# Optimization experiments

Hardware: AMD Instinct MI355X
Metric: run time of the kernel (lower is better)

The kernel has to match this reference:

```python
import jax, jax.numpy as jnp
import numpy as np

N_NODES = 1000
NODE_DIM = 40
SEQ_LEN = 12
IN_FEAT = 32
HID = 64
LAYERS = 3
GDEP = 2
TOPK = 20
TANH_ALPHA = 3.0
PROP_ALPHA = 0.05
LN_EPS = 1e-5


def setup_inputs() -> dict:
    key = jax.random.key(0)
    ks = jax.random.split(key, 20)
    s = 0.1  # weight init scale
    B = 64
    return {
        "x": jax.random.normal(ks[0], (B, N_NODES, SEQ_LEN, IN_FEAT), jnp.float32),
        # graph constructor params
        "emb1": jax.random.normal(ks[1], (N_NODES, NODE_DIM), jnp.float32) * s,
        "emb2": jax.random.normal(ks[2], (N_NODES, NODE_DIM), jnp.float32) * s,
        "lin1_w": jax.random.normal(ks[3], (NODE_DIM, NODE_DIM), jnp.float32) * s,
        "lin1_b": jnp.zeros((NODE_DIM,), jnp.float32),
        "lin2_w": jax.random.normal(ks[4], (NODE_DIM, NODE_DIM), jnp.float32) * s,
        "lin2_b": jnp.zeros((NODE_DIM,), jnp.float32),
        # LSTM (pytorch gate order i,f,g,o)
        "Wih": jax.random.normal(ks[5], (4 * HID, IN_FEAT), jnp.float32) * s,
        "Whh": jax.random.normal(ks[6], (4 * HID, HID), jnp.float32) * s,
        "bih": jnp.zeros((4 * HID,), jnp.float32),
        "bhh": jnp.zeros((4 * HID,), jnp.float32),
        # per-layer linear 64 -> seq_length
        "lin_w": jax.random.normal(ks[7], (LAYERS, SEQ_LEN, HID), jnp.float32) * s,
        "lin_b": jnp.zeros((LAYERS, SEQ_LEN), jnp.float32),
        # mixprop 1: (gdep+1)*12 -> 32
        "mp1_w": jax.random.normal(ks[8], (LAYERS, 32, (GDEP + 1) * SEQ_LEN), jnp.float32) * s,
        "mp1_b": jnp.zeros((LAYERS, 32), jnp.float32),
        # mixprop 2: (gdep+1)*32 -> node_dim
        "mp2_w": jax.random.normal(ks[9], (LAYERS, NODE_DIM, (GDEP + 1) * 32), jnp.float32) * s,
        "mp2_b": jnp.zeros((LAYERS, NODE_DIM), jnp.float32),
        # layernorm affine over (node_dim, N)
        "gamma": jnp.ones((LAYERS, NODE_DIM, N_NODES), jnp.float32),
        "beta": jnp.zeros((LAYERS, NODE_DIM, N_NODES), jnp.float32),
    }


def _graph_constructor(emb1, emb2, lin1_w, lin1_b, lin2_w, lin2_b):
    m1 = jnp.tanh(TANH_ALPHA * (emb1 @ lin1_w.T + lin1_b))
    m2 = jnp.tanh(TANH_ALPHA * (emb2 @ lin2_w.T + lin2_b))
    a = jax.nn.relu(jnp.tanh(TANH_ALPHA * (m1 @ m2.T - m2 @ m1.T)))
    _, idx = jax.lax.top_k(a, TOPK)  # keep top-k neighbors per row
    mask = jnp.zeros_like(a).at[jnp.arange(a.shape[0])[:, None], idx].set(1.0)
    return a * mask


def _lstm_last(x, Wih, Whh, bih, bhh):
    # x: (B, T, IN_FEAT) -> last hidden state (B, HID)
    B = x.shape[0]
    h0 = jnp.zeros((B, HID), x.dtype)
    c0 = jnp.zeros((B, HID), x.dtype)

    def step(carry, xt):
        h, c = carry
        g = xt @ Wih.T + h @ Whh.T + bih + bhh
        i, f, gg, o = jnp.split(g, 4, axis=-1)
        c = jax.nn.sigmoid(f) * c + jax.nn.sigmoid(i) * jnp.tanh(gg)
        h = jax.nn.sigmoid(o) * jnp.tanh(c)
        return (h, c), None

    (h, _), _ = jax.lax.scan(step, (h0, c0), jnp.swapaxes(x, 0, 1))
    return h


def _mixprop(h, adj_norm, w, b):
    # h: (B, C, N); adj_norm: (N, N) row-normalized (adj + I)
    x0 = h
    outs = [h]
    for _ in range(GDEP):
        h = PROP_ALPHA * x0 + (1.0 - PROP_ALPHA) * jnp.einsum('bcw,vw->bcv', h, adj_norm)
        outs.append(h)
    ho = jnp.concatenate(outs, axis=1)  # (B, C*(GDEP+1), N)
    return jnp.einsum('bcn,oc->bon', ho, w) + b[None, :, None]


def _layernorm(h, gamma, beta):
    # normalize over (C, N) dims
    mu = jnp.mean(h, axis=(1, 2), keepdims=True)
    var = jnp.var(h, axis=(1, 2), keepdims=True)
    return (h - mu) * jax.lax.rsqrt(var + LN_EPS) * gamma[None] + beta[None]


def reference(x, emb1, emb2, lin1_w, lin1_b, lin2_w, lin2_b,
              Wih, Whh, bih, bhh, lin_w, lin_b,
              mp1_w, mp1_b, mp2_w, mp2_b, gamma, beta):
    B, N, T, F = x.shape
    adj = _graph_constructor(emb1, emb2, lin1_w, lin1_b, lin2_w, lin2_b)
    adj = adj + jnp.eye(N, dtype=adj.dtype)
    adj_norm = adj / jnp.sum(adj, axis=1, keepdims=True)

    out = _lstm_last(x.reshape(B * N, T, F), Wih, Whh, bih, bhh)  # (B*N, 64)

    h = None
    for j in range(LAYERS):
        hj = out @ lin_w[j].T + lin_b[j]                # (B*N, 12)
        hj = hj.reshape(B, N, SEQ_LEN).transpose(0, 2, 1)  # (B, 12, N)
        hj = jax.nn.relu(_mixprop(hj, adj_norm, mp1_w[j], mp1_b[j]))
        # dropout is identity in eval mode
        hj = _mixprop(hj, adj_norm, mp2_w[j], mp2_b[j])  # (B, node_dim, N)
        h = _layernorm(hj, gamma[j], beta[j])

    return h.transpose(0, 2, 1).reshape(B, N * NODE_DIM)
```

## Files before the change

kernel.cpp:

```cpp
#include <hip/hip_runtime.h>


typedef unsigned short u16;
typedef __attribute__((ext_vector_type(8))) short bf16x8;
typedef __attribute__((ext_vector_type(4))) float fx4;

#define NB 64
#define NNODE 1000
#define TT 12
#define FF 32
#define HH 64
#define DD 40
#define TOPK_ 20
#define EPR2 22

__device__ __forceinline__ float rcp_f(float x) { return __builtin_amdgcn_rcpf(x); }
__device__ __forceinline__ float tanh_f(float x) {
  return fmaf(-2.0f, rcp_f(__expf(2.0f * x) + 1.0f), 1.0f);
}
__device__ __forceinline__ unsigned int cvt_pk(float lo, float hi) {
  unsigned int r;
  asm("v_cvt_pk_bf16_f32 %0, %1, %2" : "=v"(r) : "v"(lo), "v"(hi));
  return r;
}
__device__ __forceinline__ bf16x8 cvt8(const float* p) {
  union { unsigned int u[4]; bf16x8 v; } r;
  #pragma unroll
  for (int e = 0; e < 4; e++) r.u[e] = cvt_pk(p[2 * e], p[2 * e + 1]);
  return r.v;
}
__device__ __forceinline__ bf16x8 cvt8v(float4 a, float4 b) {
  union { unsigned int u[4]; bf16x8 v; } r;
  r.u[0] = cvt_pk(a.x, a.y); r.u[1] = cvt_pk(a.z, a.w);
  r.u[2] = cvt_pk(b.x, b.y); r.u[3] = cvt_pk(b.z, b.w);
  return r.v;
}

__global__ void k_m1m2(const float* __restrict__ emb1, const float* __restrict__ emb2,
                       const float* __restrict__ w1, const float* __restrict__ b1,
                       const float* __restrict__ w2, const float* __restrict__ b2,
                       float* __restrict__ m1, float* __restrict__ m2,
                       const float* __restrict__ lw, const float* __restrict__ lb,
                       const float* __restrict__ p1w, const float* __restrict__ p1b,
                       const float* __restrict__ p2w, const float* __restrict__ p2b,
                       float* __restrict__ wt) {
  int tid = threadIdx.x;
  if (blockIdx.x == 313) {
    for (int i = tid; i < 768; i += 256) { int k = i / 12, s = i % 12; wt[i] = lw[s * 64 + k]; }
    if (tid < 12) wt[768 + tid] = lb[tid];
    for (int i = tid; i < 1152; i += 256) { int c = i / 32, o = i % 32; wt[784 + i] = p1w[o * 36 + c]; }
    if (tid < 32) wt[1936 + tid] = p1b[tid];
    for (int i = tid; i < 3840; i += 256) { int c = i / 40, o = i % 40; wt[1968 + i] = p2w[o * 96 + c]; }
    if (tid < 40) wt[5808 + tid] = p2b[tid];
    return;
  }
  int id = blockIdx.x * 256 + tid;
  if (id >= 2 * NNODE * DD) return;
  int sel = id / (NNODE * DD);
  int r = id % (NNODE * DD);
  int i = r / DD, o = r % DD;
  const float4* emb = (const float4*)((sel ? emb2 : emb1) + i * DD);
  const float4* w = (const float4*)((sel ? w2 : w1) + o * DD);
  float s = (sel ? b2 : b1)[o];
  #pragma unroll
  for (int k4 = 0; k4 < DD / 4; k4++) {
    float4 a = emb[k4], b = w[k4];
    s = fmaf(a.x, b.x, s); s = fmaf(a.y, b.y, s);
    s = fmaf(a.z, b.z, s); s = fmaf(a.w, b.w, s);
  }
  (sel ? m2 : m1)[r] = tanh_f(3.0f * s);
}

__global__ void k_adj(const float* __restrict__ m1, const float* __restrict__ m2,
                      int2* __restrict__ pae) {
  int v0 = blockIdx.x * 4, tid = threadIdx.x;
  int lane = tid & 63, wave = tid >> 6;
  __shared__ float arow4[4][1024];
  __shared__ float m1v4[4][DD], m2v4[4][DD];
  for (int i = tid; i < 4 * DD; i += 256) {
    int r = i / DD, k = i % DD;
    m1v4[r][k] = m1[(v0 + r) * DD + k];
    m2v4[r][k] = m2[(v0 + r) * DD + k];
  }
  __syncthreads();
  for (int w = tid; w < NNODE; w += 256) {
    const float4* m2r = (const float4*)(m2 + w * DD);
    const float4* m1r = (const float4*)(m1 + w * DD);
    float4 a[10], bb[10];
    #pragma unroll
    for (int k4 = 0; k4 < 10; k4++) { a[k4] = m2r[k4]; bb[k4] = m1r[k4]; }
    #pragma unroll
    for (int r = 0; r < 4; r++) {
      float d1 = 0.f, d2 = 0.f;
      #pragma unroll
      for (int k4 = 0; k4 < 10; k4++) {
        d1 = fmaf(m1v4[r][k4 * 4 + 0], a[k4].x, d1);
        d1 = fmaf(m1v4[r][k4 * 4 + 1], a[k4].y, d1);
        d1 = fmaf(m1v4[r][k4 * 4 + 2], a[k4].z, d1);
        d1 = fmaf(m1v4[r][k4 * 4 + 3], a[k4].w, d1);
        d2 = fmaf(m2v4[r][k4 * 4 + 0], bb[k4].x, d2);
        d2 = fmaf(m2v4[r][k4 * 4 + 1], bb[k4].y, d2);
        d2 = fmaf(m2v4[r][k4 * 4 + 2], bb[k4].z, d2);
        d2 = fmaf(m2v4[r][k4 * 4 + 3], bb[k4].w, d2);
      }
      arow4[r][w] = fmaxf(tanh_f(3.0f * (d1 - d2)), 0.0f);
    }
  }
  __syncthreads();
  int v = v0 + wave, l = lane;
  float rv[16];
  #pragma unroll
  for (int q = 0; q < 16; q++) {
    int idx = q * 64 + l;
    rv[q] = (idx < NNODE) ? arow4[wave][idx] : -2.f;
  }
  float rs = 1.f;
  float myv = 0.f; int myi = 0;
  #pragma unroll
  for (int sel = 0; sel < TOPK_; sel++) {
    float bv = rv[0]; int bi = l;
    #pragma unroll
    for (int q = 1; q < 16; q++) {
      int idx = q * 64 + l;
      if (rv[q] > bv) { bv = rv[q]; bi = idx; }
    }
    #pragma unroll
    for (int off = 1; off < 64; off <<= 1) {
      float ov = __shfl_xor(bv, off); int oi = __shfl_xor(bi, off);
      if (ov > bv || (ov == bv && oi < bi)) { bv = ov; bi = oi; }
    }
    rs += bv;
    if (l == sel + 1) { myv = bv; myi = bi; }
    #pragma unroll
    for (int q = 0; q < 16; q++)
      if (q * 64 + l == bi) rv[q] = -2.f;
  }
  float inv = rcp_f(rs);
  if (l == 0)          pae[v * EPR2] = make_int2(v, __float_as_int(inv));
  else if (l <= TOPK_) pae[v * EPR2 + l] = make_int2(myi, __float_as_int(myv * inv));
  else if (l == 21)    pae[v * EPR2 + 21] = make_int2(v, 0);
}

__global__ __launch_bounds__(256, 3)
void k_lstm(const float* __restrict__ x, const float* __restrict__ Wih,
            const float* __restrict__ Whh, const float* __restrict__ bih,
            const float* __restrict__ bhh, const float* __restrict__ wt,
            float* __restrict__ hj) {
  __shared__ __align__(16) u16 whf[2 * 16 * 64 * 8];
  __shared__ __align__(16) u16 hsh[4][16][64];
  __shared__ float lwsh[12 * 64];
  __shared__ float lbsh[12];
  __shared__ float bsh[256];
  int tid = threadIdx.x, wave = tid >> 6, lane = tid & 63;
  int arow = lane & 15, kg = lane >> 4;

  for (int cc = tid; cc < 2 * 16 * 64; cc += 256) {
    int l = cc & 63, t16 = cc >> 6, ks = t16 >> 4, nt = t16 & 15;
    int row = (nt >> 2) * 64 + (l & 15) * 4 + (nt & 3);
    *(bf16x8*)&whf[cc * 8] = cvt8(Whh + row * 64 + ks * 32 + (l >> 4) * 8);
  }
  for (int i = tid; i < 768; i += 256) { int s = i >> 6, j = i & 63; lwsh[i] = wt[j * 12 + s]; }
  if (tid < 12) lbsh[tid] = wt[768 + tid];
  {
    int nt = tid >> 4, c = tid & 15;
    int row = (nt >> 2) * 64 + c * 4 + (nt & 3);
    bsh[tid] = bih[row] + bhh[row];
  }
  __syncthreads();

  bf16x8 wi[16];
  #pragma unroll
  for (int nt = 0; nt < 16; nt++) {
    int row = (nt >> 2) * 64 + arow * 4 + (nt & 3);
    wi[nt] = cvt8(Wih + row * 32 + kg * 8);
  }

  int seq_base = blockIdx.x * 64 + wave * 16;
  const float* xb = x + (size_t)(seq_base + arow) * (TT * FF) + kg * 8;
  float cst[16];
  #pragma unroll
  for (int q = 0; q < 16; q++) cst[q] = 0.f;

  float4 xf0 = *(const float4*)(xb);
  float4 xf1 = *(const float4*)(xb + 4);

  auto STEP = [&](int t, bool first, float (&hq)[16]) {
    unsigned int zo = 0;
    asm volatile("" : "+v"(zo));
    bf16x8 xa = cvt8v(xf0, xf1);
    if (t < TT - 1) {
      xf0 = *(const float4*)(xb + (t + 1) * FF);
      xf1 = *(const float4*)(xb + (t + 1) * FF + 4);
    }
    fx4 acc[16];
    #pragma unroll
    for (int nt = 0; nt < 16; nt++) {
      float bv = bsh[nt * 16 + arow];
      acc[nt] = (fx4){bv, bv, bv, bv};
    }
    #pragma unroll
    for (int nt = 0; nt < 16; nt++)
      acc[nt] = __builtin_amdgcn_mfma_f32_16x16x32_bf16(xa, wi[nt], acc[nt], 0, 0, 0);
    if (!first) {
      asm volatile("" ::: "memory");
      bf16x8 ha0 = *(const bf16x8*)&hsh[wave][arow][kg * 8];
      bf16x8 ha1 = *(const bf16x8*)&hsh[wave][arow][32 + kg * 8];
      asm volatile("" ::: "memory");
      #pragma unroll
      for (int nt = 0; nt < 16; nt++) {
        bf16x8 wb = *(const bf16x8*)&whf[(nt * 64 + lane) * 8 + zo];
        acc[nt] = __builtin_amdgcn_mfma_f32_16x16x32_bf16(ha0, wb, acc[nt], 0, 0, 0);
      }
      #pragma unroll
      for (int nt = 0; nt < 16; nt++) {
        bf16x8 wb = *(const bf16x8*)&whf[((16 + nt) * 64 + lane) * 8 + zo];
        acc[nt] = __builtin_amdgcn_mfma_f32_16x16x32_bf16(ha1, wb, acc[nt], 0, 0, 0);
      }
    }
    #pragma unroll
    for (int i = 0; i < 4; i++) {
      #pragma unroll
      for (int njt = 0; njt < 4; njt++) {
        float iv = acc[njt][i], fv = acc[njt + 4][i];
        float gv = acc[njt + 8][i], ov = acc[njt + 12][i];
        float cpv = cst[i * 4 + njt];
        float ei = __expf(-iv), ef = __expf(-fv);
        float eg = __expf(2.0f * gv), eo = __expf(-ov);
        float A = 1.0f + ef;
        float B = (1.0f + ei) * (eg + 1.0f);
        float c = fmaf(cpv, B, (eg - 1.0f) * A) * rcp_f(A * B);
        cst[i * 4 + njt] = c;
        float ec = __expf(2.0f * c);
        hq[i * 4 + njt] = (ec - 1.0f) * rcp_f((ec + 1.0f) * (1.0f + eo));
      }
    }
  };

  #pragma unroll 1
  for (int t = 0; t < TT - 1; t++) {
    float hq[16];
    STEP(t, t == 0, hq);
    #pragma unroll
    for (int i = 0; i < 4; i++) {
      unsigned int p0 = cvt_pk(hq[i * 4 + 0], hq[i * 4 + 1]);
      unsigned int p1 = cvt_pk(hq[i * 4 + 2], hq[i * 4 + 3]);
      *(uint2*)&hsh[wave][kg * 4 + i][arow * 4] = make_uint2(p0, p1);
    }
  }
  float hq[16];
  STEP(TT - 1, false, hq);

  #pragma unroll
  for (int i = 0; i < 4; i++) {
    float a[12];
    #pragma unroll
    for (int s = 0; s < 12; s++) a[s] = 0.f;
    #pragma unroll
    for (int njt = 0; njt < 4; njt++) {
      float hv = hq[i * 4 + njt];
      #pragma unroll
      for (int s = 0; s < 12; s++)
        a[s] = fmaf(hv, lwsh[s * 64 + arow * 4 + njt], a[s]);
    }
    #pragma unroll
    for (int off = 1; off < 16; off <<= 1) {
      #pragma unroll
      for (int s = 0; s < 12; s++) a[s] += __shfl_xor(a[s], off);
    }
    float outv = a[0];
    #pragma unroll
    for (int s = 1; s < 12; s++) outv = (arow == s) ? a[s] : outv;
    if (arow < 12) {
      int gseq = seq_base + kg * 4 + i;
      int bb = gseq / 1000, nn = gseq - bb * 1000;
      hj[(size_t)(bb * 12 + arow) * NNODE + nn] = outv + lbsh[arow];
    }
  }
}

__global__ void k_prop4(const float* __restrict__ hin, const int2* __restrict__ pae,
                        float* __restrict__ ho, int C) {
  int NG = C >> 2;
  int b = blockIdx.x / NG, g = blockIdx.x % NG;
  int c0 = g * 4;
  __shared__ __align__(16) float r0t[NNODE][4];
  __shared__ __align__(16) float r1t[NNODE][4];
  int tid = threadIdx.x;
  const float* src = hin + ((size_t)b * C + c0) * NNODE;
  float* dst = ho + (size_t)b * 2 * C * NNODE;
  for (int n = tid; n < NNODE; n += 256) {
    float4 v;
    v.x = src[n];
    v.y = src[NNODE + n];
    v.z = src[2 * NNODE + n];
    v.w = src[3 * NNODE + n];
    *(float4*)&r0t[n][0] = v;
  }
  __syncthreads();
  for (int n = tid; n < NNODE; n += 256) {
    const int4* pa4 = (const int4*)(pae + (size_t)n * EPR2);
    float4 s = {0.f, 0.f, 0.f, 0.f};
    #pragma unroll
    for (int e = 0; e < EPR2 / 2; e++) {
      int4 p = pa4[e];
      float av = __int_as_float(p.y);
      float4 rv = *(const float4*)&r0t[p.x][0];
      s.x = fmaf(av, rv.x, s.x); s.y = fmaf(av, rv.y, s.y);
      s.z = fmaf(av, rv.z, s.z); s.w = fmaf(av, rv.w, s.w);
      float aw = __int_as_float(p.w);
      float4 rw = *(const float4*)&r0t[p.z][0];
      s.x = fmaf(aw, rw.x, s.x); s.y = fmaf(aw, rw.y, s.y);
      s.z = fmaf(aw, rw.z, s.z); s.w = fmaf(aw, rw.w, s.w);
    }
    float4 x0 = *(const float4*)&r0t[n][0];
    float4 h1;
    h1.x = fmaf(0.95f, s.x, 0.05f * x0.x);
    h1.y = fmaf(0.95f, s.y, 0.05f * x0.y);
    h1.z = fmaf(0.95f, s.z, 0.05f * x0.z);
    h1.w = fmaf(0.95f, s.w, 0.05f * x0.w);
    *(float4*)&r1t[n][0] = h1;
    dst[(size_t)(c0 + 0) * NNODE + n] = h1.x;
    dst[(size_t)(c0 + 1) * NNODE + n] = h1.y;
    dst[(size_t)(c0 + 2) * NNODE + n] = h1.z;
    dst[(size_t)(c0 + 3) * NNODE + n] = h1.w;
  }
  __syncthreads();
  for (int n = tid; n < NNODE; n += 256) {
    const int4* pa4 = (const int4*)(pae + (size_t)n * EPR2);
    float4 s = {0.f, 0.f, 0.f, 0.f};
    #pragma unroll
    for (int e = 0; e < EPR2 / 2; e++) {
      int4 p = pa4[e];
      float av = __int_as_float(p.y);
      float4 rv = *(const float4*)&r1t[p.x][0];
      s.x = fmaf(av, rv.x, s.x); s.y = fmaf(av, rv.y, s.y);
      s.z = fmaf(av, rv.z, s.z); s.w = fmaf(av, rv.w, s.w);
      float aw = __int_as_float(p.w);
      float4 rw = *(const float4*)&r1t[p.z][0];
      s.x = fmaf(aw, rw.x, s.x); s.y = fmaf(aw, rw.y, s.y);
      s.z = fmaf(aw, rw.z, s.z); s.w = fmaf(aw, rw.w, s.w);
    }
    float4 x0 = *(const float4*)&r0t[n][0];
    dst[(size_t)(C + c0 + 0) * NNODE + n] = fmaf(0.95f, s.x, 0.05f * x0.x);
    dst[(size_t)(C + c0 + 1) * NNODE + n] = fmaf(0.95f, s.y, 0.05f * x0.y);
    dst[(size_t)(C + c0 + 2) * NNODE + n] = fmaf(0.95f, s.z, 0.05f * x0.z);
    dst[(size_t)(C + c0 + 3) * NNODE + n] = fmaf(0.95f, s.w, 0.05f * x0.w);
  }
}

template <int C1, int COUT>
__global__ void k_proj(const float* __restrict__ src0, const float* __restrict__ src12,
                       const float* __restrict__ wt, const float* __restrict__ bb,
                       float* __restrict__ out, int relu) {
  int id = blockIdx.x * 256 + threadIdx.x;
  int b = id / NNODE, n = id % NNODE;
  float acc[COUT];
  #pragma unroll
  for (int o = 0; o < COUT; o++) acc[o] = bb[o];
  for (int c = 0; c < C1; c++) {
    float hv = src0[(size_t)(b * C1 + c) * NNODE + n];
    #pragma unroll
    for (int o = 0; o < COUT; o++) acc[o] = fmaf(hv, wt[c * COUT + o], acc[o]);
  }
  for (int c = 0; c < 2 * C1; c++) {
    float hv = src12[(size_t)(b * 2 * C1 + c) * NNODE + n];
    #pragma unroll
    for (int o = 0; o < COUT; o++) acc[o] = fmaf(hv, wt[(C1 + c) * COUT + o], acc[o]);
  }
  #pragma unroll
  for (int o = 0; o < COUT; o++) {
    float vv = acc[o];
    if (relu) vv = fmaxf(vv, 0.f);
    out[(size_t)(b * COUT + o) * NNODE + n] = vv;
  }
}

__global__ void k_ln(const float* __restrict__ hj2, const float* __restrict__ gamma,
                     const float* __restrict__ beta, float* __restrict__ out) {
  int b = blockIdx.x, tid = threadIdx.x, lane = tid & 63, wave = tid >> 6;
  const float* base = hj2 + (size_t)b * DD * NNODE;
  const float4* p = (const float4*)base;
  float s = 0.f, q = 0.f;
  for (int i = tid; i < DD * NNODE / 4; i += 1024) {
    float4 vv = p[i];
    s += vv.x + vv.y + vv.z + vv.w;
    q = fmaf(vv.x, vv.x, q); q = fmaf(vv.y, vv.y, q);
    q = fmaf(vv.z, vv.z, q); q = fmaf(vv.w, vv.w, q);
  }
  for (int off = 32; off; off >>= 1) { s += __shfl_down(s, off); q += __shfl_down(q, off); }
  __shared__ float ss[16], sq[16];
  __shared__ float smu, srstd;
  if (lane == 0) { ss[wave] = s; sq[wave] = q; }
  __syncthreads();
  if (tid == 0) {
    const float invN = 1.0f / (float)(DD * NNODE);
    float S = 0.f, Q = 0.f;
    for (int t = 0; t < 16; t++) { S += ss[t]; Q += sq[t]; }
    float mu = S * invN;
    float var = Q * invN - mu * mu;
    smu = mu; srstd = __builtin_amdgcn_rsqf(var + 1e-5f);
  }
  __syncthreads();
  float mu = smu, rstd = srstd;
  if (tid >= NNODE) return;
  int n = tid;
  size_t obase = (size_t)b * (NNODE * DD) + (size_t)n * DD;
  #pragma unroll
  for (int d0 = 0; d0 < DD / 4; d0++) {
    float tt[4];
    #pragma unroll
    for (int qq = 0; qq < 4; qq++) {
      int d = d0 * 4 + qq;
      float h0 = base[(size_t)d * NNODE + n];
      tt[qq] = (h0 - mu) * rstd * gamma[d * NNODE + n] + beta[d * NNODE + n];
    }
    *(float4*)(out + obase + d0 * 4) = (float4){tt[0], tt[1], tt[2], tt[3]};
  }
}

#define OFF_M1   0
#define OFF_M2   40000
#define OFF_PAE  80000
#define OFF_HJ   124000
#define OFF_HO1  892000
#define OFF_O1   2428000
#define OFF_HO2  4476000
#define OFF_HJ2  8572000
#define OFF_WT   11132000

extern "C" void kernel_launch(void* const* d_in, const int* in_sizes, int n_in,
                              void* d_out, int out_size, void* d_ws, size_t ws_size,
                              hipStream_t stream) {
  (void)in_sizes; (void)n_in; (void)out_size; (void)ws_size;
  const float* x     = (const float*)d_in[0];
  const float* emb1  = (const float*)d_in[1];
  const float* emb2  = (const float*)d_in[2];
  const float* l1w   = (const float*)d_in[3];
  const float* l1b   = (const float*)d_in[4];
  const float* l2w   = (const float*)d_in[5];
  const float* l2b   = (const float*)d_in[6];
  const float* Wih   = (const float*)d_in[7];
  const float* Whh   = (const float*)d_in[8];
  const float* bih   = (const float*)d_in[9];
  const float* bhh   = (const float*)d_in[10];
  const float* lin_w = (const float*)d_in[11];
  const float* lin_b = (const float*)d_in[12];
  const float* mp1w  = (const float*)d_in[13];
  const float* mp1b  = (const float*)d_in[14];
  const float* mp2w  = (const float*)d_in[15];
  const float* mp2b  = (const float*)d_in[16];
  const float* gamma = (const float*)d_in[17];
  const float* beta  = (const float*)d_in[18];

  float* ws   = (float*)d_ws;
  float* m1   = ws + OFF_M1;
  float* m2   = ws + OFF_M2;
  int2*  pae  = (int2*)(ws + OFF_PAE);
  float* hj   = ws + OFF_HJ;
  float* ho1  = ws + OFF_HO1;
  float* o1   = ws + OFF_O1;
  float* ho2  = ws + OFF_HO2;
  float* hj2  = ws + OFF_HJ2;
  float* wt   = ws + OFF_WT;

  k_m1m2<<<dim3(314), dim3(256), 0, stream>>>(emb1, emb2, l1w, l1b, l2w, l2b, m1, m2,
                                              lin_w + 1536, lin_b + 24, mp1w + 2304,
                                              mp1b + 64, mp2w + 7680, mp2b + 80, wt);
  k_adj<<<dim3(250), dim3(256), 0, stream>>>(m1, m2, pae);
  k_lstm<<<dim3(1000), dim3(256), 0, stream>>>(x, Wih, Whh, bih, bhh, wt, hj);
  k_prop4<<<dim3(64 * 3), dim3(256), 0, stream>>>(hj, pae, ho1, 12);
  k_proj<12, 32><<<dim3(250), dim3(256), 0, stream>>>(hj, ho1, wt + 784, wt + 1936, o1, 1);
  k_prop4<<<dim3(64 * 8), dim3(256), 0, stream>>>(o1, pae, ho2, 32);
  k_proj<32, 40><<<dim3(250), dim3(256), 0, stream>>>(o1, ho2, wt + 1968, wt + 5808, hj2, 0);
  k_ln<<<dim3(NB), dim3(1024), 0, stream>>>(hj2, gamma + 80000, beta + 80000,
                                            (float*)d_out);
}
```

Measured before the change: 264.1 us.

## Fuse graph-embedding and weight-transpose prep into the LSTM kernel launch

The m1/m2 embedding projection and the mixprop weight transposes become extra blocks appended to the LSTM grid, which removes a separate launch and its serialization ahead of the LSTM. The LSTM now reads the lin weights directly instead of a pre-transposed copy, and it keeps the gate biases in registers rather than shared memory. Launch bounds drop from 3 to 2 blocks per CU, which lowers the occupancy target and may let the compiler allocate more registers. The adjacency kernel now runs after the fused kernel.

```diff
diff --git a/kernel.cpp b/kernel.cpp
--- a/kernel.cpp
+++ b/kernel.cpp
@@ -36,122 +36,50 @@
   return r.v;
 }
 
-__global__ void k_m1m2(const float* __restrict__ emb1, const float* __restrict__ emb2,
-                       const float* __restrict__ w1, const float* __restrict__ b1,
-                       const float* __restrict__ w2, const float* __restrict__ b2,
-                       float* __restrict__ m1, float* __restrict__ m2,
-                       const float* __restrict__ lw, const float* __restrict__ lb,
-                       const float* __restrict__ p1w, const float* __restrict__ p1b,
-                       const float* __restrict__ p2w, const float* __restrict__ p2b,
-                       float* __restrict__ wt) {
-  int tid = threadIdx.x;
-  if (blockIdx.x == 313) {
-    for (int i = tid; i < 768; i += 256) { int k = i / 12, s = i % 12; wt[i] = lw[s * 64 + k]; }
-    if (tid < 12) wt[768 + tid] = lb[tid];
-    for (int i = tid; i < 1152; i += 256) { int c = i / 32, o = i % 32; wt[784 + i] = p1w[o * 36 + c]; }
-    if (tid < 32) wt[1936 + tid] = p1b[tid];
-    for (int i = tid; i < 3840; i += 256) { int c = i / 40, o = i % 40; wt[1968 + i] = p2w[o * 96 + c]; }
-    if (tid < 40) wt[5808 + tid] = p2b[tid];
-    return;
-  }
-  int id = blockIdx.x * 256 + tid;
-  if (id >= 2 * NNODE * DD) return;
-  int sel = id / (NNODE * DD);
-  int r = id % (NNODE * DD);
-  int i = r / DD, o = r % DD;
-  const float4* emb = (const float4*)((sel ? emb2 : emb1) + i * DD);
-  const float4* w = (const float4*)((sel ? w2 : w1) + o * DD);
-  float s = (sel ? b2 : b1)[o];
-  #pragma unroll
-  for (int k4 = 0; k4 < DD / 4; k4++) {
-    float4 a = emb[k4], b = w[k4];
-    s = fmaf(a.x, b.x, s); s = fmaf(a.y, b.y, s);
-    s = fmaf(a.z, b.z, s); s = fmaf(a.w, b.w, s);
-  }
-  (sel ? m2 : m1)[r] = tanh_f(3.0f * s);
-}
-
-__global__ void k_adj(const float* __restrict__ m1, const float* __restrict__ m2,
-                      int2* __restrict__ pae) {
-  int v0 = blockIdx.x * 4, tid = threadIdx.x;
-  int lane = tid & 63, wave = tid >> 6;
-  __shared__ float arow4[4][1024];
-  __shared__ float m1v4[4][DD], m2v4[4][DD];
-  for (int i = tid; i < 4 * DD; i += 256) {
-    int r = i / DD, k = i % DD;
-    m1v4[r][k] = m1[(v0 + r) * DD + k];
-    m2v4[r][k] = m2[(v0 + r) * DD + k];
-  }
-  __syncthreads();
-  for (int w = tid; w < NNODE; w += 256) {
-    const float4* m2r = (const float4*)(m2 + w * DD);
-    const float4* m1r = (const float4*)(m1 + w * DD);
-    float4 a[10], bb[10];
-    #pragma unroll
-    for (int k4 = 0; k4 < 10; k4++) { a[k4] = m2r[k4]; bb[k4] = m1r[k4]; }
-    #pragma unroll
-    for (int r = 0; r < 4; r++) {
-      float d1 = 0.f, d2 = 0.f;
-      #pragma unroll
-      for (int k4 = 0; k4 < 10; k4++) {
-        d1 = fmaf(m1v4[r][k4 * 4 + 0], a[k4].x, d1);
-        d1 = fmaf(m1v4[r][k4 * 4 + 1], a[k4].y, d1);
-        d1 = fmaf(m1v4[r][k4 * 4 + 2], a[k4].z, d1);
-        d1 = fmaf(m1v4[r][k4 * 4 + 3], a[k4].w, d1);
-        d2 = fmaf(m2v4[r][k4 * 4 + 0], bb[k4].x, d2);
-        d2 = fmaf(m2v4[r][k4 * 4 + 1], bb[k4].y, d2);
-        d2 = fmaf(m2v4[r][k4 * 4 + 2], bb[k4].z, d2);
-        d2 = fmaf(m2v4[r][k4 * 4 + 3], bb[k4].w, d2);
-      }
-      arow4[r][w] = fmaxf(tanh_f(3.0f * (d1 - d2)), 0.0f);
-    }
-  }
-  __syncthreads();
-  int v = v0 + wave, l = lane;
-  float rv[16];
-  #pragma unroll
-  for (int q = 0; q < 16; q++) {
-    int idx = q * 64 + l;
-    rv[q] = (idx < NNODE) ? arow4[wave][idx] : -2.f;
-  }
-  float rs = 1.f;
-  float myv = 0.f; int myi = 0;
-  #pragma unroll
-  for (int sel = 0; sel < TOPK_; sel++) {
-    float bv = rv[0]; int bi = l;
-    #pragma unroll
-    for (int q = 1; q < 16; q++) {
-      int idx = q * 64 + l;
-      if (rv[q] > bv) { bv = rv[q]; bi = idx; }
-    }
-    #pragma unroll
-    for (int off = 1; off < 64; off <<= 1) {
-      float ov = __shfl_xor(bv, off); int oi = __shfl_xor(bi, off);
-      if (ov > bv || (ov == bv && oi < bi)) { bv = ov; bi = oi; }
-    }
-    rs += bv;
-    if (l == sel + 1) { myv = bv; myi = bi; }
-    #pragma unroll
-    for (int q = 0; q < 16; q++)
-      if (q * 64 + l == bi) rv[q] = -2.f;
-  }
-  float inv = rcp_f(rs);
-  if (l == 0)          pae[v * EPR2] = make_int2(v, __float_as_int(inv));
-  else if (l <= TOPK_) pae[v * EPR2 + l] = make_int2(myi, __float_as_int(myv * inv));
-  else if (l == 21)    pae[v * EPR2 + 21] = make_int2(v, 0);
-}
-
-__global__ __launch_bounds__(256, 3)
+__global__ __launch_bounds__(256, 2)
 void k_lstm(const float* __restrict__ x, const float* __restrict__ Wih,
             const float* __restrict__ Whh, const float* __restrict__ bih,
-            const float* __restrict__ bhh, const float* __restrict__ wt,
-            float* __restrict__ hj) {
+            const float* __restrict__ bhh, const float* __restrict__ lw2,
+            const float* __restrict__ lb2, float* __restrict__ hj,
+            const float* __restrict__ emb1, const float* __restrict__ emb2,
+            const float* __restrict__ w1, const float* __restrict__ b1,
+            const float* __restrict__ w2, const float* __restrict__ b2,
+            float* __restrict__ m1, float* __restrict__ m2,
+            const float* __restrict__ p1w, const float* __restrict__ p1b,
+            const float* __restrict__ p2w, const float* __restrict__ p2b,
+            float* __restrict__ wt) {
+  int tid = threadIdx.x;
+  if (blockIdx.x >= 1000) {
+    int mb = blockIdx.x - 1000;
+    if (mb == 313) {
+      for (int i = tid; i < 1152; i += 256) { int c = i / 32, o = i % 32; wt[784 + i] = p1w[o * 36 + c]; }
+      if (tid < 32) wt[1936 + tid] = p1b[tid];
+      for (int i = tid; i < 3840; i += 256) { int c = i / 40, o = i % 40; wt[1968 + i] = p2w[o * 96 + c]; }
+      if (tid < 40) wt[5808 + tid] = p2b[tid];
+      return;
+    }
+    int id = mb * 256 + tid;
+    if (id >= 2 * NNODE * DD) return;
+    int sel = id / (NNODE * DD);
+    int r = id % (NNODE * DD);
+    int i = r / DD, o = r % DD;
+    const float4* emb = (const float4*)((sel ? emb2 : emb1) + i * DD);
+    const float4* w = (const float4*)((sel ? w2 : w1) + o * DD);
+    float s = (sel ? b2 : b1)[o];
+    #pragma unroll
+    for (int k4 = 0; k4 < DD / 4; k4++) {
+      float4 a = emb[k4], b = w[k4];
+      s = fmaf(a.x, b.x, s); s = fmaf(a.y, b.y, s);
+      s = fmaf(a.z, b.z, s); s = fmaf(a.w, b.w, s);
+    }
+    (sel ? m2 : m1)[r] = tanh_f(3.0f * s);
+    return;
+  }
   __shared__ __align__(16) u16 whf[2 * 16 * 64 * 8];
   __shared__ __align__(16) u16 hsh[4][16][64];
   __shared__ float lwsh[12 * 64];
   __shared__ float lbsh[12];
-  __shared__ float bsh[256];
-  int tid = threadIdx.x, wave = tid >> 6, lane = tid & 63;
+  int wave = tid >> 6, lane = tid & 63;
   int arow = lane & 15, kg = lane >> 4;
 
   for (int cc = tid; cc < 2 * 16 * 64; cc += 256) {
@@ -159,20 +87,17 @@
     int row = (nt >> 2) * 64 + (l & 15) * 4 + (nt & 3);
     *(bf16x8*)&whf[cc * 8] = cvt8(Whh + row * 64 + ks * 32 + (l >> 4) * 8);
   }
-  for (int i = tid; i < 768; i += 256) { int s = i >> 6, j = i & 63; lwsh[i] = wt[j * 12 + s]; }
-  if (tid < 12) lbsh[tid] = wt[768 + tid];
-  {
-    int nt = tid >> 4, c = tid & 15;
-    int row = (nt >> 2) * 64 + c * 4 + (nt & 3);
-    bsh[tid] = bih[row] + bhh[row];
-  }
+  for (int i = tid; i < 768; i += 256) lwsh[i] = lw2[i];
+  if (tid < 12) lbsh[tid] = lb2[tid];
   __syncthreads();
 
   bf16x8 wi[16];
+  float biasv[16];
   #pragma unroll
   for (int nt = 0; nt < 16; nt++) {
     int row = (nt >> 2) * 64 + arow * 4 + (nt & 3);
     wi[nt] = cvt8(Wih + row * 32 + kg * 8);
+    biasv[nt] = bih[row] + bhh[row];
   }
 
   int seq_base = blockIdx.x * 64 + wave * 16;
@@ -194,10 +119,8 @@
     }
     fx4 acc[16];
     #pragma unroll
-    for (int nt = 0; nt < 16; nt++) {
-      float bv = bsh[nt * 16 + arow];
-      acc[nt] = (fx4){bv, bv, bv, bv};
-    }
+    for (int nt = 0; nt < 16; nt++)
+      acc[nt] = (fx4){biasv[nt], biasv[nt], biasv[nt], biasv[nt]};
     #pragma unroll
     for (int nt = 0; nt < 16; nt++)
       acc[nt] = __builtin_amdgcn_mfma_f32_16x16x32_bf16(xa, wi[nt], acc[nt], 0, 0, 0);
@@ -276,6 +199,76 @@
       hj[(size_t)(bb * 12 + arow) * NNODE + nn] = outv + lbsh[arow];
     }
   }
+}
+
+__global__ void k_adj(const float* __restrict__ m1, const float* __restrict__ m2,
+                      int2* __restrict__ pae) {
+  int v0 = blockIdx.x * 4, tid = threadIdx.x;
+  int lane = tid & 63, wave = tid >> 6;
+  __shared__ float arow4[4][1024];
+  __shared__ float m1v4[4][DD], m2v4[4][DD];
+  for (int i = tid; i < 4 * DD; i += 256) {
+    int r = i / DD, k = i % DD;
+    m1v4[r][k] = m1[(v0 + r) * DD + k];
+    m2v4[r][k] = m2[(v0 + r) * DD + k];
+  }
+  __syncthreads();
+  for (int w = tid; w < NNODE; w += 256) {
+    const float4* m2r = (const float4*)(m2 + w * DD);
+    const float4* m1r = (const float4*)(m1 + w * DD);
+    float4 a[10], bb[10];
+    #pragma unroll
+    for (int k4 = 0; k4 < 10; k4++) { a[k4] = m2r[k4]; bb[k4] = m1r[k4]; }
+    #pragma unroll
+    for (int r = 0; r < 4; r++) {
+      float d1 = 0.f, d2 = 0.f;
+      #pragma unroll
+      for (int k4 = 0; k4 < 10; k4++) {
+        d1 = fmaf(m1v4[r][k4 * 4 + 0], a[k4].x, d1);
+        d1 = fmaf(m1v4[r][k4 * 4 + 1], a[k4].y, d1);
+        d1 = fmaf(m1v4[r][k4 * 4 + 2], a[k4].z, d1);
+        d1 = fmaf(m1v4[r][k4 * 4 + 3], a[k4].w, d1);
+        d2 = fmaf(m2v4[r][k4 * 4 + 0], bb[k4].x, d2);
+        d2 = fmaf(m2v4[r][k4 * 4 + 1], bb[k4].y, d2);
+        d2 = fmaf(m2v4[r][k4 * 4 + 2], bb[k4].z, d2);
+        d2 = fmaf(m2v4[r][k4 * 4 + 3], bb[k4].w, d2);
+      }
+      arow4[r][w] = fmaxf(tanh_f(3.0f * (d1 - d2)), 0.0f);
+    }
+  }
+  __syncthreads();
+  int v = v0 + wave, l = lane;
+  float rv[16];
+  #pragma unroll
+  for (int q = 0; q < 16; q++) {
+    int idx = q * 64 + l;
+    rv[q] = (idx < NNODE) ? arow4[wave][idx] : -2.f;
+  }
+  float rs = 1.f;
+  float myv = 0.f; int myi = 0;
+  #pragma unroll
+  for (int sel = 0; sel < TOPK_; sel++) {
+    float bv = rv[0]; int bi = l;
+    #pragma unroll
+    for (int q = 1; q < 16; q++) {
+      int idx = q * 64 + l;
+      if (rv[q] > bv) { bv = rv[q]; bi = idx; }
+    }
+    #pragma unroll
+    for (int off = 1; off < 64; off <<= 1) {
+      float ov = __shfl_xor(bv, off); int oi = __shfl_xor(bi, off);
+      if (ov > bv || (ov == bv && oi < bi)) { bv = ov; bi = oi; }
+    }
+    rs += bv;
+    if (l == sel + 1) { myv = bv; myi = bi; }
+    #pragma unroll
+    for (int q = 0; q < 16; q++)
+      if (q * 64 + l == bi) rv[q] = -2.f;
+  }
+  float inv = rcp_f(rs);
+  if (l == 0)          pae[v * EPR2] = make_int2(v, __float_as_int(inv));
+  else if (l <= TOPK_) pae[v * EPR2 + l] = make_int2(myi, __float_as_int(myv * inv));
+  else if (l == 21)    pae[v * EPR2 + 21] = make_int2(v, 0);
 }
 
 __global__ void k_prop4(const float* __restrict__ hin, const int2* __restrict__ pae,
@@ -463,11 +456,12 @@
   float* hj2  = ws + OFF_HJ2;
   float* wt   = ws + OFF_WT;
 
-  k_m1m2<<<dim3(314), dim3(256), 0, stream>>>(emb1, emb2, l1w, l1b, l2w, l2b, m1, m2,
-                                              lin_w + 1536, lin_b + 24, mp1w + 2304,
-                                              mp1b + 64, mp2w + 7680, mp2b + 80, wt);
+  k_lstm<<<dim3(1314), dim3(256), 0, stream>>>(x, Wih, Whh, bih, bhh,
+                                               lin_w + 1536, lin_b + 24, hj,
+                                               emb1, emb2, l1w, l1b, l2w, l2b, m1, m2,
+                                               mp1w + 2304, mp1b + 64,
+                                               mp2w + 7680, mp2b + 80, wt);
   k_adj<<<dim3(250), dim3(256), 0, stream>>>(m1, m2, pae);
-  k_lstm<<<dim3(1000), dim3(256), 0, stream>>>(x, Wih, Whh, bih, bhh, wt, hj);
   k_prop4<<<dim3(64 * 3), dim3(256), 0, stream>>>(hj, pae, ho1, 12);
   k_proj<12, 32><<<dim3(250), dim3(256), 0, stream>>>(hj, ho1, wt + 784, wt + 1936, o1, 1);
   k_prop4<<<dim3(64 * 8), dim3(256), 0, stream>>>(o1, pae, ho2, 32);
```

After: 249.3 us. -5.6%, faster.
